# Kernel tuning notes

Measured on AMD Instinct MI355X. Metric: run time of the kernel, lower is better.

## Reference

```python
import jax, jax.numpy as jnp
import numpy as np
import math

B, N, M, Lx = 8, 32, 16, 32
D, TE_DIM, IN_DIM, TT = 64, 16, 17, 63   # hid_dim, te_dim, 1+te_dim, hid_dim-1
H, DH, NL = 4, 16, 2
TAU, DELTA = 60.0, 300.0                 # tau, 5 minutes in seconds
P = B * N * M


def _ln(x, g, b):
    mu = x.mean(-1, keepdims=True)
    v = ((x - mu) ** 2).mean(-1, keepdims=True)
    return (x - mu) / jnp.sqrt(v + 1e-5) * g + b


def _time_bias():
    idx = jnp.arange(M)
    dist = jnp.abs(idx[:, None] - idx[None, :]).astype(jnp.float32) * DELTA
    return jnp.log(jnp.exp(-dist / TAU) + 1e-12)


def _pos_enc():
    pos = jnp.arange(M, dtype=jnp.float32)[:, None]
    div = jnp.exp(jnp.arange(0, D, 2, dtype=jnp.float32) * (-math.log(10000.0) / D))
    pe = jnp.zeros((M, D))
    pe = pe.at[:, 0::2].set(jnp.sin(pos * div))
    pe = pe.at[:, 1::2].set(jnp.cos(pos * div))
    return pe


def _heads(t):   # (b, m, D) -> (b, H, m, DH)
    b, m, _ = t.shape
    return t.reshape(b, m, H, DH).transpose(0, 2, 1, 3)


def _merge(t):   # (b, H, m, DH) -> (b, m, D)
    b, _, m, _ = t.shape
    return t.transpose(0, 2, 1, 3).reshape(b, m, D)


def _patch_gattn(x, pm, qw, qb, kw, kb, vw, vb, ow, ob, tbias):
    q, k, v = _heads(x @ qw.T + qb), _heads(x @ kw.T + kb), _heads(x @ vw.T + vb)
    a = jnp.einsum('bhqd,bhkd->bhqk', q, k) / math.sqrt(DH) + tbias[None, None]
    a = jnp.where((pm == 0.0)[:, None, None, :], -1e9, a)
    out = _merge(jnp.einsum('bhqk,bhkd->bhqd', jax.nn.softmax(a, -1), v))
    return (out @ ow.T + ob) * pm[..., None]


def _mha(q_in, kv_in, in_w, in_b, ow, ob, kpm=None):
    wq, wk, wv = in_w[:D], in_w[D:2 * D], in_w[2 * D:]
    bq, bk, bv = in_b[:D], in_b[D:2 * D], in_b[2 * D:]
    q = _heads(q_in @ wq.T + bq)
    k = _heads(kv_in @ wk.T + bk)
    v = _heads(kv_in @ wv.T + bv)
    a = jnp.einsum('bhqd,bhkd->bhqk', q, k) / math.sqrt(DH)
    if kpm is not None:
        a = jnp.where(kpm[:, None, None, :], -1e9, a)
    out = _merge(jnp.einsum('bhqk,bhkd->bhqd', jax.nn.softmax(a, -1), v))
    return out @ ow.T + ob


def _forward(x, mask, ttcn_w1, ttcn_b1, ttcn_w2, ttcn_b2, ttcn_w3, ttcn_b3, t_bias,
             ga_qw, ga_qb, ga_kw, ga_kb, ga_vw, ga_vb, ga_ow, ga_ob,
             tf_in_w, tf_in_b, tf_out_w, tf_out_b, tf_ln1_g, tf_ln1_b, tf_ln2_g, tf_ln2_b,
             tf_fw1, tf_fb1, tf_fw2, tf_fb2,
             q_embed, cls_in_w, cls_in_b, cls_out_w, cls_out_b, logit_w, logit_b):
    m = mask.astype(x.dtype)                          # (P, Lx, 1)
    # --- TTCN: per-sample dynamic filter generation + masked seq-softmax agg ---
    h = jax.nn.relu(x @ ttcn_w1.T + ttcn_b1)
    h = jax.nn.relu(h @ ttcn_w2.T + ttcn_b2)
    filt = h @ ttcn_w3.T + ttcn_b3                    # (P, Lx, IN_DIM*TT)
    filt = filt * m + (1.0 - m) * (-1e8)
    fs = jax.nn.softmax(filt, axis=1).reshape(P, Lx, TT, IN_DIM)
    h_t = jax.nn.relu(jnp.einsum('pli,plti->pt', x, fs) + t_bias)   # (P, TT)
    mask_patch = (m.sum(axis=1) > 0).astype(x.dtype)  # (P, 1)
    xp = jnp.concatenate([h_t, mask_patch], -1).reshape(B, N, M, D)
    pm = mask_patch.reshape(B, N, M)
    tbias = _time_bias()
    pe = _pos_enc()
    xc = xp
    for l in range(NL):
        if l > 0:
            x_last = xc
        xb = xc.reshape(B * N, M, D)
        pmb = pm.reshape(B * N, M)
        xb = xb + _patch_gattn(xb, pmb, ga_qw[l], ga_qb[l], ga_kw[l], ga_kb[l],
                               ga_vw[l], ga_vb[l], ga_ow[l], ga_ob[l], tbias)
        xb = xb + pe[None]
        # post-norm TransformerEncoderLayer (tf_layer = 1, no attn mask, eval mode)
        attn = _mha(xb, xb, tf_in_w[l], tf_in_b[l], tf_out_w[l], tf_out_b[l])
        xb = _ln(xb + attn, tf_ln1_g[l], tf_ln1_b[l])
        ff = jax.nn.relu(xb @ tf_fw1[l].T + tf_fb1[l]) @ tf_fw2[l].T + tf_fb2[l]
        xb = _ln(xb + ff, tf_ln2_g[l], tf_ln2_b[l])
        xc = xb.reshape(B, N, M, D)
        if l > 0:
            xc = x_last + xc
    x_seq = xc.mean(axis=1)                            # (B, M, D)
    kpm = ~((pm > 0).any(axis=1))                      # (B, M), True = padded
    qs = jnp.broadcast_to(q_embed[None], (B, 5, D))
    z = _mha(qs, x_seq, cls_in_w, cls_in_b, cls_out_w, cls_out_b, kpm=kpm)
    return (z @ logit_w.T + logit_b)[..., 0]           # (B, 5)


def setup_inputs() -> dict:
    key = jax.random.key(0)
    ks = iter(jax.random.split(key, 64))
    def rn(shape, s=0.1):
        return jax.random.normal(next(ks), shape, jnp.float32) * s
    inp = {
        'x': jax.random.normal(next(ks), (P, Lx, IN_DIM), jnp.float32),
        'mask': jax.random.randint(next(ks), (P, Lx, 1), 0, 2, jnp.int32),
        'ttcn_w1': rn((TT, IN_DIM)), 'ttcn_b1': jnp.zeros((TT,)),
        'ttcn_w2': rn((TT, TT)), 'ttcn_b2': jnp.zeros((TT,)),
        'ttcn_w3': rn((IN_DIM * TT, TT)), 'ttcn_b3': jnp.zeros((IN_DIM * TT,)),
        't_bias': rn((1, TT)),
        'ga_qw': rn((NL, D, D)), 'ga_qb': jnp.zeros((NL, D)),
        'ga_kw': rn((NL, D, D)), 'ga_kb': jnp.zeros((NL, D)),
        'ga_vw': rn((NL, D, D)), 'ga_vb': jnp.zeros((NL, D)),
        'ga_ow': rn((NL, D, D)), 'ga_ob': jnp.zeros((NL, D)),
        'tf_in_w': rn((NL, 3 * D, D)), 'tf_in_b': jnp.zeros((NL, 3 * D)),
        'tf_out_w': rn((NL, D, D)), 'tf_out_b': jnp.zeros((NL, D)),
        'tf_ln1_g': jnp.ones((NL, D)), 'tf_ln1_b': jnp.zeros((NL, D)),
        'tf_ln2_g': jnp.ones((NL, D)), 'tf_ln2_b': jnp.zeros((NL, D)),
        'tf_fw1': rn((NL, 2048, D)), 'tf_fb1': jnp.zeros((NL, 2048)),
        'tf_fw2': rn((NL, D, 2048)), 'tf_fb2': jnp.zeros((NL, D)),
        'q_embed': rn((5, D), 1.0),
        'cls_in_w': rn((3 * D, D)), 'cls_in_b': jnp.zeros((3 * D,)),
        'cls_out_w': rn((D, D)), 'cls_out_b': jnp.zeros((D,)),
        'logit_w': rn((1, D)), 'logit_b': jnp.zeros((1,)),
    }
    return inp


def reference(x, mask, ttcn_w1, ttcn_b1, ttcn_w2, ttcn_b2, ttcn_w3, ttcn_b3, t_bias,
              ga_qw, ga_qb, ga_kw, ga_kb, ga_vw, ga_vb, ga_ow, ga_ob,
              tf_in_w, tf_in_b, tf_out_w, tf_out_b, tf_ln1_g, tf_ln1_b, tf_ln2_g, tf_ln2_b,
              tf_fw1, tf_fb1, tf_fw2, tf_fb2,
              q_embed, cls_in_w, cls_in_b, cls_out_w, cls_out_b, logit_w, logit_b):
    return _forward(x, mask, ttcn_w1, ttcn_b1, ttcn_w2, ttcn_b2, ttcn_w3, ttcn_b3, t_bias,
                    ga_qw, ga_qb, ga_kw, ga_kb, ga_vw, ga_vb, ga_ow, ga_ob,
                    tf_in_w, tf_in_b, tf_out_w, tf_out_b, tf_ln1_g, tf_ln1_b, tf_ln2_g, tf_ln2_b,
                    tf_fw1, tf_fb1, tf_fw2, tf_fb2,
                    q_embed, cls_in_w, cls_in_b, cls_out_w, cls_out_b, logit_w, logit_b)
```

## Files before the change

### kernel.cpp

```cpp
#include <hip/hip_runtime.h>
#include <hip/hip_bf16.h>
#include <math.h>

#define B_  8
#define N_  32
#define M_  16
#define LX  32
#define D_  64
#define IN_DIM_ 17
#define TT_ 63
#define H_  4
#define DH_ 16
#define P_TOT 4096
#define BN_ 256
#define FF_ 2048

#define FRAG_TOT 83200
#define OFF_INW  2048
#define OFF_OUTW 3584
#define OFF_FW1  4096
#define OFF_FW2  20480

typedef unsigned short ushort_t;
typedef __attribute__((ext_vector_type(8))) short short8;
typedef __attribute__((ext_vector_type(4))) float floatx4;

#define MFMA16(a,b,c) __builtin_amdgcn_mfma_f32_16x16x32_bf16((a),(b),(c),0,0,0)

__device__ __forceinline__ float fast_exp2(float x){
#if __has_builtin(__builtin_amdgcn_exp2f)
  return __builtin_amdgcn_exp2f(x);
#else
  return __expf(x * 0.6931471805599453f);
#endif
}
__device__ __forceinline__ float fast_rcp(float x){
#if __has_builtin(__builtin_amdgcn_rcpf)
  return __builtin_amdgcn_rcpf(x);
#else
  return 1.0f / x;
#endif
}

__device__ __forceinline__ ushort_t f2bf(float f){
  unsigned u = __float_as_uint(f);
  u += 0x7FFFu + ((u >> 16) & 1u);
  return (ushort_t)(u >> 16);
}
__device__ __forceinline__ float bf2f(ushort_t h){ return __uint_as_float(((unsigned)h) << 16); }

__device__ __forceinline__ uint4 pack8(const ushort_t* h){
  uint4 u;
  u.x = (unsigned)h[0] | ((unsigned)h[1] << 16);
  u.y = (unsigned)h[2] | ((unsigned)h[3] << 16);
  u.z = (unsigned)h[4] | ((unsigned)h[5] << 16);
  u.w = (unsigned)h[6] | ((unsigned)h[7] << 16);
  return u;
}

__device__ __forceinline__ void split8(const float* r, short8& hi, short8& lo){
  #pragma unroll
  for (int j = 0; j < 8; ++j){
    float v = r[j];
    ushort_t h = f2bf(v);
    ushort_t l2 = f2bf(v - bf2f(h));
    hi[j] = (short)h; lo[j] = (short)l2;
  }
}
__device__ __forceinline__ uint4 cvt8(const float* r){
  ushort_t hh[8];
  #pragma unroll
  for (int j = 0; j < 8; ++j) hh[j] = f2bf(r[j]);
  return pack8(hh);
}
__device__ __forceinline__ short8 cvt8s(const float* r){
  union { uint4 u4; short8 s8; } cv;
  cv.u4 = cvt8(r);
  return cv.s8;
}

__device__ __forceinline__ floatx4 mm3(short8 ah, short8 al, short8 bh, short8 bl, floatx4 c){
  c = MFMA16(ah, bh, c); c = MFMA16(ah, bl, c); c = MFMA16(al, bh, c); return c;
}

__device__ __forceinline__ float dot64(const float* __restrict__ a, const float* __restrict__ w){
  const float4* a4 = (const float4*)a;
  const float4* w4 = (const float4*)w;
  float acc = 0.f;
  #pragma unroll
  for (int k = 0; k < 16; ++k){ float4 x = a4[k], y = w4[k];
    acc += x.x*y.x + x.y*y.y + x.z*y.z + x.w*y.w; }
  return acc;
}
__device__ __forceinline__ float dot16(const float* __restrict__ a, const float* __restrict__ b){
  const float4* a4 = (const float4*)a; const float4* b4 = (const float4*)b;
  float acc = 0.f;
  #pragma unroll
  for (int k = 0; k < 4; ++k){ float4 x = a4[k], y = b4[k];
    acc += x.x*y.x + x.y*y.y + x.z*y.z + x.w*y.w; }
  return acc;
}

__device__ __forceinline__ void packA68(const float* buf, short8* fA, int tid){
  if (tid < 128){
    int ln = tid & 63, ks = tid >> 6;
    const float* r = buf + (ln & 15)*68 + ks*32 + ((ln >> 4) & 3)*8;
    short8 hi, lo; split8(r, hi, lo);
    fA[tid] = hi; fA[128 + tid] = lo;
  }
}

__global__ __launch_bounds__(256) void prep_kernel(
    const float* __restrict__ w1, const float* __restrict__ w2, const float* __restrict__ w3,
    const float* __restrict__ gqw, const float* __restrict__ gkw,
    const float* __restrict__ gvw, const float* __restrict__ gow,
    const float* __restrict__ inw, const float* __restrict__ outw,
    const float* __restrict__ fw1, const float* __restrict__ fw2,
    uint4* __restrict__ fr)
{
  int s = blockIdx.x*256 + threadIdx.x;
  if (s >= FRAG_TOT) return;
  const float* src; int Nr, Kr, KS, rel; int w3seg = 0, noLo = 0;
  if (s < 256)      { src = w1; Nr=63;  Kr=17; KS=1; rel = s; noLo = 1; }
  else if (s < 768) { src = w2; Nr=63;  Kr=63; KS=2; rel = s-256; noLo = 1; }
  else if (s < 9472){ src = w3; Nr=1071;Kr=63; KS=2; rel = s-768; w3seg = 1; noLo = 1; }
  else {
    int t = s - 9472, l = t / 36864, r2 = t - l*36864;
    if (r2 < 512)        { src = gqw + l*4096;   Nr=64;  Kr=64;   KS=2;  rel = r2; }
    else if (r2 < 1024)  { src = gkw + l*4096;   Nr=64;  Kr=64;   KS=2;  rel = r2-512; }
    else if (r2 < 1536)  { src = gvw + l*4096;   Nr=64;  Kr=64;   KS=2;  rel = r2-1024; }
    else if (r2 < 2048)  { src = gow + l*4096;   Nr=64;  Kr=64;   KS=2;  rel = r2-1536; }
    else if (r2 < 3584)  { src = inw + l*12288;  Nr=192; Kr=64;   KS=2;  rel = r2-2048; }
    else if (r2 < 4096)  { src = outw + l*4096;  Nr=64;  Kr=64;   KS=2;  rel = r2-3584; }
    else if (r2 < 20480) { src = fw1 + l*131072; Nr=2048;Kr=64;   KS=2;  rel = r2-4096; noLo = 1; }
    else                 { src = fw2 + l*131072; Nr=64;  Kr=2048; KS=64; rel = r2-20480; noLo = 1; }
  }
  int lane = rel & 63, tmp = rel >> 6;
  int ks = tmp % KS, nt = tmp / KS;
  int kb = ks*32 + ((lane >> 4) & 3)*8;
  int n, validn;
  if (w3seg){
    int i = nt >> 2, tq = nt & 3;
    int t = tq*16 + (lane & 15);
    n = t*17 + i;
    validn = (t < 63);
  } else {
    n = nt*16 + (lane & 15);
    validn = (n < Nr);
  }
  float v[8];
  #pragma unroll
  for (int j = 0; j < 8; ++j){
    v[j] = (validn && (kb + j) < Kr) ? src[n*Kr + kb + j] : 0.f;
    if (w3seg){
      if ((kb + j) == 63) v[j] = 1.0f;
      v[j] *= 1.4426950408889634f;
    }
  }
  ushort_t hh[8];
  #pragma unroll
  for (int j = 0; j < 8; ++j) hh[j] = f2bf(v[j]);
  fr[s] = pack8(hh);
  if (!noLo){
    ushort_t ll[8];
    #pragma unroll
    for (int j = 0; j < 8; ++j) ll[j] = f2bf(v[j] - bf2f(hh[j]));
    fr[FRAG_TOT + s] = pack8(ll);
  }
}

__global__ __launch_bounds__(256) void ttcn_kernel(
    const float* __restrict__ x, const int* __restrict__ mask,
    const float* __restrict__ b1, const float* __restrict__ b2,
    const float* __restrict__ tb,
    const short8* __restrict__ w1bhi,
    const short8* __restrict__ w2bhi,
    const short8* __restrict__ w3bhi,
    float* __restrict__ xp, float* __restrict__ pm)
{
  __shared__ __align__(16) char pool[16512];
  float*    xs    = (float*)(pool + 0);
  float*    xst   = (float*)(pool + 2560);
  int*      cmap  = (int*)  (pool + 5008);
  float*    xsumv = (float*)(pool + 5136);
  int*      Vp    = (int*)  (pool + 5204);
  short8*   xfhi  = (short8*)(pool + 5216);
  ushort_t* h1t   = (ushort_t*)(pool + 7264);
  ushort_t* h2t   = (ushort_t*)(pool + 11872);

  const int p = blockIdx.x, tid = threadIdx.x;
  const int lane = tid & 63, wvi = tid >> 6;
  const int nidx = lane & 15, quad = lane >> 4;

  for (int idx = tid; idx < LX*IN_DIM_; idx += 256){
    int l = (idx * 3856) >> 16;
    int i = idx - l*17;
    xs[l*20 + i] = x[p*(LX*IN_DIM_) + idx];
  }
  if (tid < 64){
    int mv = (tid < 32) ? mask[p*LX + tid] : 0;
    unsigned long long bal = __ballot(mv != 0);
    if (tid < 32) cmap[tid] = 0;
    int pos = __popcll(bal & ((1ull << tid) - 1ull));
    if (mv != 0) cmap[pos] = tid;
    if (tid == 0) *Vp = (int)__popcll(bal);
  }
  __syncthreads();
  const int V   = *Vp;
  const int two = (V > 16);

  if (tid < 128){
    int mt = tid >> 6;
    if (mt == 0 || two){
      int lc = cmap[mt*16 + nidx];
      float r[8];
      #pragma unroll
      for (int j = 0; j < 8; ++j){
        int k = quad*8 + j;
        r[j] = (k < IN_DIM_) ? xs[lc*20 + k] : 0.f;
      }
      ((uint4*)xfhi)[tid] = cvt8(r);
    }
  } else {
    if (tid < 128 + IN_DIM_){
      int i = tid - 128;
      float s = 0.f;
      #pragma unroll
      for (int l = 0; l < LX; ++l) s += xs[l*20 + i];
      xsumv[i] = s;
    }
    if (two){
      for (int idx = tid - 128; idx < 544; idx += 128){
        int i = idx >> 5, cl = idx & 31;
        xst[i*36 + cl] = xs[cmap[cl]*20 + i];
      }
    } else {
      for (int idx = tid - 128; idx < 272; idx += 128){
        int i = idx >> 4, cl = idx & 15;
        xst[i*36 + cl] = xs[cmap[cl]*20 + i];
      }
    }
  }
  __syncthreads();

  {
    short8 axh0 = xfhi[lane];
    short8 bh = w1bhi[wvi*64 + lane];
    floatx4 a0 = {0.f,0.f,0.f,0.f};
    a0 = MFMA16(axh0, bh, a0);
    int t = wvi*16 + nidx;
    float bb = (t < TT_) ? b1[t] : 0.f;
    if (two){
      short8 axh1 = xfhi[64 + lane];
      floatx4 a1 = {0.f,0.f,0.f,0.f};
      a1 = MFMA16(axh1, bh, a1);
      #pragma unroll
      for (int r = 0; r < 4; ++r)
        h1t[(16+quad*4+r)*72 + t] = f2bf(fmaxf(a1[r] + bb, 0.f));
    }
    #pragma unroll
    for (int r = 0; r < 4; ++r)
      h1t[(quad*4+r)*72 + t] = f2bf(fmaxf(a0[r] + bb, 0.f));
  }
  __syncthreads();

  {
    short8 bh0 = w2bhi[(wvi*2+0)*64 + lane];
    short8 bh1 = w2bhi[(wvi*2+1)*64 + lane];
    short8 a00 = *(const short8*)((const char*)h1t + (nidx*72 + quad*8)*2);
    short8 a01 = *(const short8*)((const char*)h1t + (nidx*72 + 32 + quad*8)*2);
    floatx4 a0 = {0.f,0.f,0.f,0.f};
    a0 = MFMA16(a00, bh0, a0); a0 = MFMA16(a01, bh1, a0);
    int t = wvi*16 + nidx;
    float bb = (t < TT_) ? b2[t] : 0.f;
    if (two){
      short8 a10 = *(const short8*)((const char*)h1t + ((16+nidx)*72 + quad*8)*2);
      short8 a11 = *(const short8*)((const char*)h1t + ((16+nidx)*72 + 32 + quad*8)*2);
      floatx4 a1 = {0.f,0.f,0.f,0.f};
      a1 = MFMA16(a10, bh0, a1); a1 = MFMA16(a11, bh1, a1);
      #pragma unroll
      for (int r = 0; r < 4; ++r)
        h2t[(16+quad*4+r)*72 + t] = f2bf(fmaxf(a1[r] + bb, 0.f));
    }
    #pragma unroll
    for (int r = 0; r < 4; ++r)
      h2t[(quad*4+r)*72 + t] = f2bf(fmaxf(a0[r] + bb, 0.f));
  }
  __syncthreads();

  {
    short8 ah0[2], ah1[2];
    #pragma unroll
    for (int ks = 0; ks < 2; ++ks)
      ah0[ks] = *(const short8*)((const char*)h2t + (nidx*72 + ks*32 + quad*8)*2);
    if (two){
      #pragma unroll
      for (int ks = 0; ks < 2; ++ks)
        ah1[ks] = *(const short8*)((const char*)h2t + ((16+nidx)*72 + ks*32 + quad*8)*2);
    }
    if (quad == 3){
      if (two) ah1[1][7] = (short)((16 + nidx >= V) ? f2bf(-1e8f) : (ushort_t)0);
      else     ah0[1][7] = (short)((nidx >= V)      ? f2bf(-1e8f) : (ushort_t)0);
    }
    const int t_out = wvi*16 + nidx;
    const int rA = quad*4;
    float acc_t = 0.f;
    short8 nbh0 = w3bhi[(wvi*2+0)*64 + lane];
    short8 nbh1 = w3bhi[(wvi*2+1)*64 + lane];
    if (two){
      for (int it = 0; it < 17; ++it){
        short8 bh0 = nbh0, bh1 = nbh1;
        if (it < 16){
          int nt = wvi + it*4 + 4;
          nbh0 = w3bhi[(nt*2+0)*64 + lane];
          nbh1 = w3bhi[(nt*2+1)*64 + lane];
        }
        floatx4 a0 = {0.f,0.f,0.f,0.f}, a1 = {0.f,0.f,0.f,0.f};
        a0 = MFMA16(ah0[0], bh0, a0); a0 = MFMA16(ah0[1], bh1, a0);
        a1 = MFMA16(ah1[0], bh0, a1); a1 = MFMA16(ah1[1], bh1, a1);

        const float4 xA = *(const float4*)(xst + it*36 + rA);
        const float4 xB = *(const float4*)(xst + it*36 + rA + 16);
        float den0 = 0.f, den1 = 0.f, num0 = 0.f, num1 = 0.f;
        float e;
        e = fast_exp2(a0[0]); den0 += e; num0 = fmaf(e, xA.x, num0);
        e = fast_exp2(a0[1]); den0 += e; num0 = fmaf(e, xA.y, num0);
        e = fast_exp2(a0[2]); den0 += e; num0 = fmaf(e, xA.z, num0);
        e = fast_exp2(a0[3]); den0 += e; num0 = fmaf(e, xA.w, num0);
        e = fast_exp2(a1[0]); den1 += e; num1 = fmaf(e, xB.x, num1);
        e = fast_exp2(a1[1]); den1 += e; num1 = fmaf(e, xB.y, num1);
        e = fast_exp2(a1[2]); den1 += e; num1 = fmaf(e, xB.z, num1);
        e = fast_exp2(a1[3]); den1 += e; num1 = fmaf(e, xB.w, num1);
        float den = den0 + den1, num = num0 + num1;
        den += __shfl_xor(den, 16, 64); den += __shfl_xor(den, 32, 64);
        num += __shfl_xor(num, 16, 64); num += __shfl_xor(num, 32, 64);
        float res = (den > 0.f) ? num * fast_rcp(den) : xsumv[it] * (1.f/32.f);
        acc_t += res;
      }
    } else {
      for (int it = 0; it < 17; ++it){
        short8 bh0 = nbh0, bh1 = nbh1;
        if (it < 16){
          int nt = wvi + it*4 + 4;
          nbh0 = w3bhi[(nt*2+0)*64 + lane];
          nbh1 = w3bhi[(nt*2+1)*64 + lane];
        }
        floatx4 a0 = {0.f,0.f,0.f,0.f};
        a0 = MFMA16(ah0[0], bh0, a0); a0 = MFMA16(ah0[1], bh1, a0);

        const float4 xA = *(const float4*)(xst + it*36 + rA);
        float den = 0.f, num = 0.f, e;
        e = fast_exp2(a0[0]); den += e; num = fmaf(e, xA.x, num);
        e = fast_exp2(a0[1]); den += e; num = fmaf(e, xA.y, num);
        e = fast_exp2(a0[2]); den += e; num = fmaf(e, xA.z, num);
        e = fast_exp2(a0[3]); den += e; num = fmaf(e, xA.w, num);
        den += __shfl_xor(den, 16, 64); den += __shfl_xor(den, 32, 64);
        num += __shfl_xor(num, 16, 64); num += __shfl_xor(num, 32, 64);
        float res = (den > 0.f) ? num * fast_rcp(den) : xsumv[it] * (1.f/32.f);
        acc_t += res;
      }
    }
    if (quad == 0 && t_out < TT_)
      xp[p*D_ + t_out] = fmaxf(acc_t + tb[t_out], 0.f);
  }
  if (tid == 0){
    float mp = (V > 0) ? 1.f : 0.f;
    xp[p*D_ + TT_] = mp;
    pm[p] = mp;
  }
}

__global__ __launch_bounds__(512) void layer12_kernel(
    const float* __restrict__ xin, const float* __restrict__ pm,
    const short8* __restrict__ frS,
    const float* __restrict__ gqb, const float* __restrict__ gkb,
    const float* __restrict__ gvb, const float* __restrict__ gob,
    const float* __restrict__ inb, const float* __restrict__ outb,
    const float* __restrict__ ln1g, const float* __restrict__ ln1b,
    const float* __restrict__ fb1, const float* __restrict__ fb2,
    const float* __restrict__ ln2g, const float* __restrict__ ln2b,
    float* __restrict__ xout)
{
  __shared__ __align__(16) float xb[16*68];
  __shared__ __align__(16) float xb2[16*68];
  __shared__ __align__(16) float q_[16*68];
  __shared__ __align__(16) float k_[16*68];
  __shared__ __align__(16) float v_[16*68];
  __shared__ __align__(16) float ao[16*68];
  __shared__ __align__(16) float ss[1024];
  __shared__ __align__(16) short8 fragA[256];
  __shared__ __align__(16) float hbuf[8*16*36];
  __shared__ __align__(16) float part[8*16*68];
  __shared__ __align__(16) float pe_t[1024];
  __shared__ float tbt[16];
  __shared__ float pmv[16], mur[16], rvr[16];

  const int bn = blockIdx.x, tid = threadIdx.x;
  const int lane = tid & 63, wvi = tid >> 6;
  const int nidx = lane & 15, quad = lane >> 4;
  const float* xin_p = xin + bn*1024;

  for (int o = tid; o < 1024; o += 512) xb[(o>>6)*68 + (o&63)] = xin_p[o];
  if (tid < 16) pmv[tid] = pm[bn*16 + tid];
  for (int o = tid; o < 1024; o += 512){
    int tok = o >> 6, d = o & 63;
    float div = __expf((float)(d & ~1) * (-0.14391156831212793f));
    float arg = (float)tok * div;
    pe_t[o] = (d & 1) ? cosf(arg) : sinf(arg);
  }
  if (tid >= 32 && tid < 48) tbt[tid-32] = logf(expf(-5.0f*(float)(tid-32)) + 1e-12f);
  __syncthreads();

  for (int l = 0; l < 2; ++l){
    const int lbase = 9472 + l*36864;
    const float* gqbL = gqb + l*64;  const float* gkbL = gkb + l*64;
    const float* gvbL = gvb + l*64;  const float* gobL = gob + l*64;
    const float* inbL = inb + l*192; const float* outbL = outb + l*64;
    const float* ln1gL = ln1g + l*64; const float* ln1bL = ln1b + l*64;
    const float* fb1L = fb1 + l*2048; const float* fb2L = fb2 + l*64;
    const float* ln2gL = ln2g + l*64; const float* ln2bL = ln2b + l*64;

    float xres[2];
    #pragma unroll
    for (int kk2 = 0; kk2 < 2; ++kk2){
      int o = tid + kk2*512;
      xres[kk2] = xb[(o>>6)*68 + (o&63)];
    }

    short8 gU0[4], gU1[4], mU0[4], mU1[4], ob4[4];
    {
      int b0 = lbase + wvi*128;
      gU0[0] = frS[b0 + lane];       gU0[1] = frS[FRAG_TOT + b0 + lane];
      gU0[2] = frS[b0 + 64 + lane];  gU0[3] = frS[FRAG_TOT + b0 + 64 + lane];
      int m0 = lbase + OFF_INW + wvi*128;
      mU0[0] = frS[m0 + lane];       mU0[1] = frS[FRAG_TOT + m0 + lane];
      mU0[2] = frS[m0 + 64 + lane];  mU0[3] = frS[FRAG_TOT + m0 + 64 + lane];
      if (wvi < 4){
        int b1 = lbase + (wvi+8)*128;
        gU1[0] = frS[b1 + lane];       gU1[1] = frS[FRAG_TOT + b1 + lane];
        gU1[2] = frS[b1 + 64 + lane];  gU1[3] = frS[FRAG_TOT + b1 + 64 + lane];
        int m1 = lbase + OFF_INW + (wvi+8)*128;
        mU1[0] = frS[m1 + lane];       mU1[1] = frS[FRAG_TOT + m1 + lane];
        mU1[2] = frS[m1 + 64 + lane];  mU1[3] = frS[FRAG_TOT + m1 + 64 + lane];
        int bo = lbase + 1536 + wvi*128;
        ob4[0] = frS[bo + lane];       ob4[1] = frS[FRAG_TOT + bo + lane];
        ob4[2] = frS[bo + 64 + lane];  ob4[3] = frS[FRAG_TOT + bo + 64 + lane];
      }
    }

    packA68(xb, fragA, tid);
    __syncthreads();
    {
      short8 axh0 = fragA[lane], axh1 = fragA[64+lane];
      short8 axl0 = fragA[128+lane], axl1 = fragA[192+lane];
      {
        int u = wvi;
        floatx4 c = {0.f,0.f,0.f,0.f};
        c = mm3(axh0, axl0, gU0[0], gU0[1], c);
        c = mm3(axh1, axl1, gU0[2], gU0[3], c);
        int sel = u >> 2, d = (u & 3)*16 + nidx;
        float bb = (sel == 0 ? gqbL : gkbL)[d];
        float* dst = (sel == 0 ? q_ : k_);
        #pragma unroll
        for (int r = 0; r < 4; ++r) dst[(quad*4+r)*68 + d] = c[r] + bb;
      }
      if (wvi < 4){
        int u = wvi + 8;
        floatx4 c = {0.f,0.f,0.f,0.f};
        c = mm3(axh0, axl0, gU1[0], gU1[1], c);
        c = mm3(axh1, axl1, gU1[2], gU1[3], c);
        int d = (u & 3)*16 + nidx;
        float bb = gvbL[d];
        #pragma unroll
        for (int r = 0; r < 4; ++r) v_[(quad*4+r)*68 + d] = c[r] + bb;
      }
    }
    __syncthreads();
    {
      int row = tid >> 3;
      int h = row >> 4, qm = row & 15;
      int km0 = (tid & 7) * 2;
      float s2[2];
      #pragma unroll
      for (int j = 0; j < 2; ++j){
        int km = km0 + j;
        float acc = dot16(q_ + qm*68 + h*16, k_ + km*68 + h*16);
        int dd = qm - km; if (dd < 0) dd = -dd;
        acc = acc * 0.25f + tbt[dd];
        if (pmv[km] == 0.f) acc = -1e9f;
        s2[j] = acc;
      }
      float mx = fmaxf(s2[0], s2[1]);
      mx = fmaxf(mx, __shfl_xor(mx, 1, 64));
      mx = fmaxf(mx, __shfl_xor(mx, 2, 64));
      mx = fmaxf(mx, __shfl_xor(mx, 4, 64));
      float e2[2], se = 0.f;
      #pragma unroll
      for (int j = 0; j < 2; ++j){ e2[j] = __expf(s2[j]-mx); se += e2[j]; }
      se += __shfl_xor(se, 1, 64);
      se += __shfl_xor(se, 2, 64);
      se += __shfl_xor(se, 4, 64);
      float inv = fast_rcp(se);
      #pragma unroll
      for (int j = 0; j < 2; ++j) ss[row*16 + km0 + j] = e2[j]*inv;
    }
    __syncthreads();
    for (int o = tid; o < 1024; o += 512){
      int m = o >> 6, d = o & 63, h = d >> 4;
      float acc = 0.f;
      #pragma unroll
      for (int km = 0; km < 16; ++km) acc += ss[h*256 + m*16 + km] * v_[km*68 + d];
      ao[m*68 + d] = acc;
    }
    __syncthreads();
    packA68(ao, fragA, tid);
    __syncthreads();
    if (wvi < 4){
      short8 axh0 = fragA[lane], axh1 = fragA[64+lane];
      short8 axl0 = fragA[128+lane], axl1 = fragA[192+lane];
      floatx4 c = {0.f,0.f,0.f,0.f};
      c = mm3(axh0, axl0, ob4[0], ob4[1], c);
      c = mm3(axh1, axl1, ob4[2], ob4[3], c);
      int d = wvi*16 + nidx;
      float bb = gobL[d];
      #pragma unroll
      for (int r = 0; r < 4; ++r){
        int tok = quad*4 + r;
        xb[tok*68 + d] += (c[r] + bb) * pmv[tok] + pe_t[tok*64 + d];
      }
    }
    __syncthreads();

    short8 mob[4], f1c[4], f2c[4];
    if (wvi < 4){
      int base = lbase + OFF_OUTW + wvi*128;
      mob[0] = frS[base + lane];       mob[1] = frS[FRAG_TOT + base + lane];
      mob[2] = frS[base + 64 + lane];  mob[3] = frS[FRAG_TOT + base + 64 + lane];
    }
    {
      int f1base = lbase + OFF_FW1, f2base = lbase + OFF_FW2;
      #pragma unroll
      for (int t2 = 0; t2 < 2; ++t2){
        int sb = f1base + ((wvi*16+t2)*2)*64 + lane;
        f1c[t2*2+0] = frS[sb];
        f1c[t2*2+1] = frS[sb + 64];
      }
      #pragma unroll
      for (int ntd = 0; ntd < 4; ++ntd)
        f2c[ntd] = frS[f2base + (ntd*64 + wvi*8)*64 + lane];
    }

    packA68(xb, fragA, tid);
    __syncthreads();
    {
      short8 axh0 = fragA[lane], axh1 = fragA[64+lane];
      short8 axl0 = fragA[128+lane], axl1 = fragA[192+lane];
      {
        int u = wvi;
        floatx4 c = {0.f,0.f,0.f,0.f};
        c = mm3(axh0, axl0, mU0[0], mU0[1], c);
        c = mm3(axh1, axl1, mU0[2], mU0[3], c);
        int sel = u >> 2, d = (u & 3)*16 + nidx;
        float bb = inbL[u*16 + nidx];
        float* dst = (sel == 0 ? q_ : k_);
        #pragma unroll
        for (int r = 0; r < 4; ++r) dst[(quad*4+r)*68 + d] = c[r] + bb;
      }
      if (wvi < 4){
        int u = wvi + 8;
        floatx4 c = {0.f,0.f,0.f,0.f};
        c = mm3(axh0, axl0, mU1[0], mU1[1], c);
        c = mm3(axh1, axl1, mU1[2], mU1[3], c);
        int d = (u & 3)*16 + nidx;
        float bb = inbL[u*16 + nidx];
        #pragma unroll
        for (int r = 0; r < 4; ++r) v_[(quad*4+r)*68 + d] = c[r] + bb;
      }
    }
    __syncthreads();
    {
      int row = tid >> 3;
      int h = row >> 4, qm = row & 15;
      int km0 = (tid & 7) * 2;
      float s2[2];
      #pragma unroll
      for (int j = 0; j < 2; ++j)
        s2[j] = 0.25f * dot16(q_ + qm*68 + h*16, k_ + (km0+j)*68 + h*16);
      float mx = fmaxf(s2[0], s2[1]);
      mx = fmaxf(mx, __shfl_xor(mx, 1, 64));
      mx = fmaxf(mx, __shfl_xor(mx, 2, 64));
      mx = fmaxf(mx, __shfl_xor(mx, 4, 64));
      float e2[2], se = 0.f;
      #pragma unroll
      for (int j = 0; j < 2; ++j){ e2[j] = __expf(s2[j]-mx); se += e2[j]; }
      se += __shfl_xor(se, 1, 64);
      se += __shfl_xor(se, 2, 64);
      se += __shfl_xor(se, 4, 64);
      float inv = fast_rcp(se);
      #pragma unroll
      for (int j = 0; j < 2; ++j) ss[row*16 + km0 + j] = e2[j]*inv;
    }
    __syncthreads();
    for (int o = tid; o < 1024; o += 512){
      int m = o >> 6, d = o & 63, h = d >> 4;
      float acc = 0.f;
      #pragma unroll
      for (int km = 0; km < 16; ++km) acc += ss[h*256 + m*16 + km] * v_[km*68 + d];
      ao[m*68 + d] = acc;
    }
    __syncthreads();
    packA68(ao, fragA, tid);
    __syncthreads();
    if (wvi < 4){
      short8 axh0 = fragA[lane], axh1 = fragA[64+lane];
      short8 axl0 = fragA[128+lane], axl1 = fragA[192+lane];
      floatx4 c = {0.f,0.f,0.f,0.f};
      c = mm3(axh0, axl0, mob[0], mob[1], c);
      c = mm3(axh1, axl1, mob[2], mob[3], c);
      int d = wvi*16 + nidx;
      float bb = outbL[d];
      #pragma unroll
      for (int r = 0; r < 4; ++r) xb[(quad*4+r)*68 + d] += c[r] + bb;
    }
    __syncthreads();

    if (tid < 64){
      int row = tid >> 2, seg = tid & 3;
      const float* rp = xb + row*68 + seg*16;
      float s = 0.f;
      #pragma unroll
      for (int j = 0; j < 16; ++j) s += rp[j];
      s += __shfl_xor(s, 1, 64); s += __shfl_xor(s, 2, 64);
      float mu = s * (1.f/64.f);
      float v = 0.f;
      #pragma unroll
      for (int j = 0; j < 16; ++j){ float t = rp[j]-mu; v += t*t; }
      v += __shfl_xor(v, 1, 64); v += __shfl_xor(v, 2, 64);
      if (seg == 0){ mur[row] = mu; rvr[row] = rsqrtf(v*(1.f/64.f) + 1e-5f); }
    }
    __syncthreads();
    for (int o = tid; o < 1024; o += 512){
      int m = o >> 6, d = o & 63;
      xb2[m*68 + d] = (xb[m*68 + d] - mur[m]) * rvr[m] * ln1gL[d] + ln1bL[d];
    }
    __syncthreads();
    packA68(xb2, fragA, tid);
    __syncthreads();

    {
      const int w = wvi;
      const int f1base = lbase + OFF_FW1, f2base = lbase + OFF_FW2;
      short8 axh0 = fragA[lane], axh1 = fragA[64 + lane];
      floatx4 y0 = {0.f,0.f,0.f,0.f}, y1 = y0, y2 = y0, y3 = y0;
      float* hw = hbuf + w*576;

      short8 f1n[4], f2n[4];
      for (int it = 0; it < 8; ++it){
        int ntA = w*16 + it*2;
        floatx4 hA = {0.f,0.f,0.f,0.f}, hB = hA;
        hA = MFMA16(axh0, f1c[0], hA); hA = MFMA16(axh1, f1c[1], hA);
        hB = MFMA16(axh0, f1c[2], hB); hB = MFMA16(axh1, f1c[3], hB);
        float bbA = fb1L[ntA*16 + nidx], bbB = fb1L[ntA*16 + 16 + nidx];
        #pragma unroll
        for (int r = 0; r < 4; ++r){
          hw[(quad*4+r)*36 + nidx]      = fmaxf(hA[r] + bbA, 0.f);
          hw[(quad*4+r)*36 + 16 + nidx] = fmaxf(hB[r] + bbB, 0.f);
        }
        if (it < 7){
          int ntN = ntA + 2, kstN = w*8 + it + 1;
          #pragma unroll
          for (int t2 = 0; t2 < 2; ++t2){
            int sb = f1base + ((ntN+t2)*2)*64 + lane;
            f1n[t2*2+0] = frS[sb];
            f1n[t2*2+1] = frS[sb + 64];
          }
          #pragma unroll
          for (int ntd = 0; ntd < 4; ++ntd)
            f2n[ntd] = frS[f2base + (ntd*64 + kstN)*64 + lane];
        }
        short8 ah = cvt8s(hw + (lane & 15)*36 + quad*8);
        y0 = MFMA16(ah, f2c[0], y0);
        y1 = MFMA16(ah, f2c[1], y1);
        y2 = MFMA16(ah, f2c[2], y2);
        y3 = MFMA16(ah, f2c[3], y3);
        #pragma unroll
        for (int j = 0; j < 4; ++j){ f1c[j] = f1n[j]; f2c[j] = f2n[j]; }
      }
      #pragma unroll
      for (int r = 0; r < 4; ++r){
        int row = (quad*4 + r)*68;
        part[w*1088 + row + nidx]      = y0[r];
        part[w*1088 + row + 16 + nidx] = y1[r];
        part[w*1088 + row + 32 + nidx] = y2[r];
        part[w*1088 + row + 48 + nidx] = y3[r];
      }
    }
    __syncthreads();
    for (int o = tid; o < 1024; o += 512){
      int tok = o >> 6, d = o & 63;
      float s = xb2[tok*68 + d] + fb2L[d];
      #pragma unroll
      for (int ww = 0; ww < 8; ++ww) s += part[ww*1088 + tok*68 + d];
      xb[tok*68 + d] = s;
    }
    __syncthreads();
    if (tid < 64){
      int row = tid >> 2, seg = tid & 3;
      const float* rp = xb + row*68 + seg*16;
      float s = 0.f;
      #pragma unroll
      for (int j = 0; j < 16; ++j) s += rp[j];
      s += __shfl_xor(s, 1, 64); s += __shfl_xor(s, 2, 64);
      float mu = s * (1.f/64.f);
      float v = 0.f;
      #pragma unroll
      for (int j = 0; j < 16; ++j){ float t = rp[j]-mu; v += t*t; }
      v += __shfl_xor(v, 1, 64); v += __shfl_xor(v, 2, 64);
      if (seg == 0){ mur[row] = mu; rvr[row] = rsqrtf(v*(1.f/64.f) + 1e-5f); }
    }
    __syncthreads();
    #pragma unroll
    for (int kk2 = 0; kk2 < 2; ++kk2){
      int o = tid + kk2*512;
      int tok = o >> 6, d = o & 63;
      float vv = (xb[tok*68 + d] - mur[tok]) * rvr[tok] * ln2gL[d] + ln2bL[d];
      if (l == 0) xb[tok*68 + d] = vv;
      else        xout[bn*1024 + o] = vv + xres[kk2];
    }
    __syncthreads();
  }
}

__global__ __launch_bounds__(256) void final_kernel(
    const float* __restrict__ xc, const float* __restrict__ pm,
    const float* __restrict__ q_embed,
    const float* __restrict__ cin_w, const float* __restrict__ cin_b,
    const float* __restrict__ cout_w, const float* __restrict__ cout_b,
    const float* __restrict__ logit_w, const float* __restrict__ logit_b,
    float* __restrict__ out)
{
  const int b = blockIdx.x;
  const int tid = threadIdx.x;
  __shared__ __align__(16) float xs[M_ * D_];
  __shared__ float kpmv[M_];
  __shared__ __align__(16) float qv[5 * D_], kv[M_ * D_], vv[M_ * D_];
  __shared__ float sv[H_ * 5 * M_];
  __shared__ __align__(16) float ao[5 * D_], zv[5 * D_];

  for (int o = tid; o < M_ * D_; o += 256) {
    int m = o >> 6, d = o & 63;
    float acc = 0.f;
    #pragma unroll
    for (int n = 0; n < N_; ++n) acc += xc[(((b * N_ + n) * M_ + m) * D_) + d];
    xs[o] = acc * (1.f / 32.f);
  }
  if (tid < M_) {
    float any = 0.f;
    #pragma unroll
    for (int n = 0; n < N_; ++n) any += (pm[(b * N_ + n) * M_ + tid] > 0.f) ? 1.f : 0.f;
    kpmv[tid] = (any > 0.f) ? 0.f : 1.f;
  }
  __syncthreads();

  for (int o = tid; o < 5 * D_; o += 256) {
    int qi = o >> 6, d = o & 63;
    qv[o] = cin_b[d] + dot64(q_embed + qi * D_, cin_w + d * D_);
  }
  for (int o = tid; o < 2 * M_ * D_; o += 256) {
    int sel = o >> 10, r = o & 1023, m = r >> 6, d = r & 63;
    float acc = cin_b[D_ + sel * D_ + d] + dot64(xs + m * D_, cin_w + (D_ + sel * D_ + d) * D_);
    ((sel == 0) ? kv : vv)[r] = acc;
  }
  __syncthreads();

  for (int o = tid; o < H_ * 5 * M_; o += 256) {
    int h = o / 80, r = o % 80, qi = r >> 4, km = r & 15;
    float acc = 0.25f * dot16(qv + qi * D_ + h * DH_, kv + km * D_ + h * DH_);
    if (kpmv[km] != 0.f) acc = -1e9f;
    sv[o] = acc;
  }
  __syncthreads();
  if (tid < H_ * 5) {
    int h = tid / 5, qi = tid % 5;
    float* row = sv + h * 80 + qi * M_;
    float mx = -1e30f;
    #pragma unroll
    for (int km = 0; km < M_; ++km) mx = fmaxf(mx, row[km]);
    float se = 0.f;
    #pragma unroll
    for (int km = 0; km < M_; ++km) { float e = __expf(row[km] - mx); row[km] = e; se += e; }
    float inv = 1.f / se;
    #pragma unroll
    for (int km = 0; km < M_; ++km) row[km] *= inv;
  }
  __syncthreads();
  for (int o = tid; o < 5 * D_; o += 256) {
    int qi = o >> 6, d = o & 63, h = d >> 4;
    float acc = 0.f;
    #pragma unroll
    for (int km = 0; km < M_; ++km) acc += sv[h * 80 + qi * M_ + km] * vv[km * D_ + d];
    ao[o] = acc;
  }
  __syncthreads();
  for (int o = tid; o < 5 * D_; o += 256) {
    int qi = o >> 6, d = o & 63;
    zv[o] = cout_b[d] + dot64(ao + qi * D_, cout_w + d * D_);
  }
  __syncthreads();
  if (tid < 5) {
    float acc = logit_b[0] + dot64(zv + tid * D_, logit_w);
    out[b * 5 + tid] = acc;
  }
}

extern "C" void kernel_launch(void* const* d_in, const int* in_sizes, int n_in,
                              void* d_out, int out_size, void* d_ws, size_t ws_size,
                              hipStream_t stream) {
  const float* x       = (const float*)d_in[0];
  const int*   mask    = (const int*)  d_in[1];
  const float* ttcn_w1 = (const float*)d_in[2];
  const float* ttcn_b1 = (const float*)d_in[3];
  const float* ttcn_w2 = (const float*)d_in[4];
  const float* ttcn_b2 = (const float*)d_in[5];
  const float* ttcn_w3 = (const float*)d_in[6];
  const float* ttcn_b3 = (const float*)d_in[7];
  const float* t_bias  = (const float*)d_in[8];
  const float* ga_qw   = (const float*)d_in[9];
  const float* ga_qb   = (const float*)d_in[10];
  const float* ga_kw   = (const float*)d_in[11];
  const float* ga_kb   = (const float*)d_in[12];
  const float* ga_vw   = (const float*)d_in[13];
  const float* ga_vb   = (const float*)d_in[14];
  const float* ga_ow   = (const float*)d_in[15];
  const float* ga_ob   = (const float*)d_in[16];
  const float* tf_in_w = (const float*)d_in[17];
  const float* tf_in_b = (const float*)d_in[18];
  const float* tf_out_w= (const float*)d_in[19];
  const float* tf_out_b= (const float*)d_in[20];
  const float* tf_ln1g = (const float*)d_in[21];
  const float* tf_ln1b = (const float*)d_in[22];
  const float* tf_ln2g = (const float*)d_in[23];
  const float* tf_ln2b = (const float*)d_in[24];
  const float* tf_fw1  = (const float*)d_in[25];
  const float* tf_fb1  = (const float*)d_in[26];
  const float* tf_fw2  = (const float*)d_in[27];
  const float* tf_fb2  = (const float*)d_in[28];
  const float* q_embed = (const float*)d_in[29];
  const float* cls_in_w  = (const float*)d_in[30];
  const float* cls_in_b  = (const float*)d_in[31];
  const float* cls_out_w = (const float*)d_in[32];
  const float* cls_out_b = (const float*)d_in[33];
  const float* logit_w = (const float*)d_in[34];
  const float* logit_b = (const float*)d_in[35];
  (void)ttcn_b3;

  float* wsf  = (float*)d_ws;
  float* xp   = wsf;
  float* pmb  = wsf + P_TOT * D_;
  float* xbuf = pmb + P_TOT;
  uint4* fr   = (uint4*)(xbuf + P_TOT * D_);
  const short8* frS = (const short8*)fr;

  prep_kernel<<<325, 256, 0, stream>>>(ttcn_w1, ttcn_w2, ttcn_w3,
      ga_qw, ga_kw, ga_vw, ga_ow, tf_in_w, tf_out_w, tf_fw1, tf_fw2, fr);

  ttcn_kernel<<<P_TOT, 256, 0, stream>>>(x, mask, ttcn_b1, ttcn_b2, t_bias,
      frS + 0, frS + 256, frS + 768,
      xp, pmb);

  layer12_kernel<<<BN_, 512, 0, stream>>>(xp, pmb, frS,
      ga_qb, ga_kb, ga_vb, ga_ob, tf_in_b, tf_out_b, tf_ln1g, tf_ln1b,
      tf_fb1, tf_fb2, tf_ln2g, tf_ln2b, xbuf);

  final_kernel<<<B_, 256, 0, stream>>>(xbuf, pmb, q_embed,
                                       cls_in_w, cls_in_b, cls_out_w, cls_out_b,
                                       logit_w, logit_b, (float*)d_out);
}
```

Baseline: 229.2 us.

## Double ttcn block width to split work across wave groups; wave-level LayerNorm

The ttcn kernel now runs 512 threads per patch. Two groups of four waves split the work: in the first two layers each group handles one 16-row tile, and in the third-layer loop each group handles about half the iterations. The partial sums are combined through shared memory after an extra barrier. In layer12, both LayerNorms become per-wave 64-lane shuffle reductions over whole rows, which drops the separate mean/rstd shared-memory pass and two barriers. This adds parallelism and cuts synchronization, at the cost of idle waves when only one row tile is valid and possibly lower occupancy.

```diff
diff --git a/kernel.cpp b/kernel.cpp
--- a/kernel.cpp
+++ b/kernel.cpp
@@ -108,6 +108,13 @@
     short8 hi, lo; split8(r, hi, lo);
     fA[tid] = hi; fA[128 + tid] = lo;
   }
+}
+
+__device__ __forceinline__ float wsum64(float v){
+  v += __shfl_xor(v, 1, 64);  v += __shfl_xor(v, 2, 64);
+  v += __shfl_xor(v, 4, 64);  v += __shfl_xor(v, 8, 64);
+  v += __shfl_xor(v, 16, 64); v += __shfl_xor(v, 32, 64);
+  return v;
 }
 
 __global__ __launch_bounds__(256) void prep_kernel(
@@ -169,7 +176,7 @@
   }
 }
 
-__global__ __launch_bounds__(256) void ttcn_kernel(
+__global__ __launch_bounds__(512) void ttcn_kernel(
     const float* __restrict__ x, const int* __restrict__ mask,
     const float* __restrict__ b1, const float* __restrict__ b2,
     const float* __restrict__ tb,
@@ -187,12 +194,14 @@
   short8*   xfhi  = (short8*)(pool + 5216);
   ushort_t* h1t   = (ushort_t*)(pool + 7264);
   ushort_t* h2t   = (ushort_t*)(pool + 11872);
+  __shared__ float accp[64];
 
   const int p = blockIdx.x, tid = threadIdx.x;
   const int lane = tid & 63, wvi = tid >> 6;
+  const int w4 = wvi & 3, grp = wvi >> 2;
   const int nidx = lane & 15, quad = lane >> 4;
 
-  for (int idx = tid; idx < LX*IN_DIM_; idx += 256){
+  for (int idx = tid; idx < LX*IN_DIM_; idx += 512){
     int l = (idx * 3856) >> 16;
     int i = idx - l*17;
     xs[l*20 + i] = x[p*(LX*IN_DIM_) + idx];
@@ -230,12 +239,12 @@
       xsumv[i] = s;
     }
     if (two){
-      for (int idx = tid - 128; idx < 544; idx += 128){
+      for (int idx = tid - 128; idx < 544; idx += 384){
         int i = idx >> 5, cl = idx & 31;
         xst[i*36 + cl] = xs[cmap[cl]*20 + i];
       }
     } else {
-      for (int idx = tid - 128; idx < 272; idx += 128){
+      for (int idx = tid - 128; idx < 272; idx += 384){
         int i = idx >> 4, cl = idx & 15;
         xst[i*36 + cl] = xs[cmap[cl]*20 + i];
       }
@@ -244,13 +253,17 @@
   __syncthreads();
 
   {
-    short8 axh0 = xfhi[lane];
-    short8 bh = w1bhi[wvi*64 + lane];
-    floatx4 a0 = {0.f,0.f,0.f,0.f};
-    a0 = MFMA16(axh0, bh, a0);
-    int t = wvi*16 + nidx;
+    int t = w4*16 + nidx;
     float bb = (t < TT_) ? b1[t] : 0.f;
-    if (two){
+    short8 bh = w1bhi[w4*64 + lane];
+    if (grp == 0){
+      short8 axh0 = xfhi[lane];
+      floatx4 a0 = {0.f,0.f,0.f,0.f};
+      a0 = MFMA16(axh0, bh, a0);
+      #pragma unroll
+      for (int r = 0; r < 4; ++r)
+        h1t[(quad*4+r)*72 + t] = f2bf(fmaxf(a0[r] + bb, 0.f));
+    } else if (two){
       short8 axh1 = xfhi[64 + lane];
       floatx4 a1 = {0.f,0.f,0.f,0.f};
       a1 = MFMA16(axh1, bh, a1);
@@ -258,22 +271,23 @@
       for (int r = 0; r < 4; ++r)
         h1t[(16+quad*4+r)*72 + t] = f2bf(fmaxf(a1[r] + bb, 0.f));
     }
-    #pragma unroll
-    for (int r = 0; r < 4; ++r)
-      h1t[(quad*4+r)*72 + t] = f2bf(fmaxf(a0[r] + bb, 0.f));
   }
   __syncthreads();
 
   {
-    short8 bh0 = w2bhi[(wvi*2+0)*64 + lane];
-    short8 bh1 = w2bhi[(wvi*2+1)*64 + lane];
-    short8 a00 = *(const short8*)((const char*)h1t + (nidx*72 + quad*8)*2);
-    short8 a01 = *(const short8*)((const char*)h1t + (nidx*72 + 32 + quad*8)*2);
-    floatx4 a0 = {0.f,0.f,0.f,0.f};
-    a0 = MFMA16(a00, bh0, a0); a0 = MFMA16(a01, bh1, a0);
-    int t = wvi*16 + nidx;
+    int t = w4*16 + nidx;
     float bb = (t < TT_) ? b2[t] : 0.f;
-    if (two){
+    short8 bh0 = w2bhi[(w4*2+0)*64 + lane];
+    short8 bh1 = w2bhi[(w4*2+1)*64 + lane];
+    if (grp == 0){
+      short8 a00 = *(const short8*)((const char*)h1t + (nidx*72 + quad*8)*2);
+      short8 a01 = *(const short8*)((const char*)h1t + (nidx*72 + 32 + quad*8)*2);
+      floatx4 a0 = {0.f,0.f,0.f,0.f};
+      a0 = MFMA16(a00, bh0, a0); a0 = MFMA16(a01, bh1, a0);
+      #pragma unroll
+      for (int r = 0; r < 4; ++r)
+        h2t[(quad*4+r)*72 + t] = f2bf(fmaxf(a0[r] + bb, 0.f));
+    } else if (two){
       short8 a10 = *(const short8*)((const char*)h1t + ((16+nidx)*72 + quad*8)*2);
       short8 a11 = *(const short8*)((const char*)h1t + ((16+nidx)*72 + 32 + quad*8)*2);
       floatx4 a1 = {0.f,0.f,0.f,0.f};
@@ -282,9 +296,6 @@
       for (int r = 0; r < 4; ++r)
         h2t[(16+quad*4+r)*72 + t] = f2bf(fmaxf(a1[r] + bb, 0.f));
     }
-    #pragma unroll
-    for (int r = 0; r < 4; ++r)
-      h2t[(quad*4+r)*72 + t] = f2bf(fmaxf(a0[r] + bb, 0.f));
   }
   __syncthreads();
 
@@ -302,16 +313,16 @@
       if (two) ah1[1][7] = (short)((16 + nidx >= V) ? f2bf(-1e8f) : (ushort_t)0);
       else     ah0[1][7] = (short)((nidx >= V)      ? f2bf(-1e8f) : (ushort_t)0);
     }
-    const int t_out = wvi*16 + nidx;
+    const int it0 = grp ? 9 : 0, it1 = grp ? 17 : 9;
     const int rA = quad*4;
     float acc_t = 0.f;
-    short8 nbh0 = w3bhi[(wvi*2+0)*64 + lane];
-    short8 nbh1 = w3bhi[(wvi*2+1)*64 + lane];
+    short8 nbh0 = w3bhi[((w4 + it0*4)*2+0)*64 + lane];
+    short8 nbh1 = w3bhi[((w4 + it0*4)*2+1)*64 + lane];
     if (two){
-      for (int it = 0; it < 17; ++it){
+      for (int it = it0; it < it1; ++it){
         short8 bh0 = nbh0, bh1 = nbh1;
-        if (it < 16){
-          int nt = wvi + it*4 + 4;
+        if (it + 1 < 17){
+          int nt = w4 + it*4 + 4;
           nbh0 = w3bhi[(nt*2+0)*64 + lane];
           nbh1 = w3bhi[(nt*2+1)*64 + lane];
         }
@@ -338,10 +349,10 @@
         acc_t += res;
       }
     } else {
-      for (int it = 0; it < 17; ++it){
+      for (int it = it0; it < it1; ++it){
         short8 bh0 = nbh0, bh1 = nbh1;
-        if (it < 16){
-          int nt = wvi + it*4 + 4;
+        if (it + 1 < 17){
+          int nt = w4 + it*4 + 4;
           nbh0 = w3bhi[(nt*2+0)*64 + lane];
           nbh1 = w3bhi[(nt*2+1)*64 + lane];
         }
@@ -360,8 +371,13 @@
         acc_t += res;
       }
     }
-    if (quad == 0 && t_out < TT_)
-      xp[p*D_ + t_out] = fmaxf(acc_t + tb[t_out], 0.f);
+    if (grp == 1 && quad == 0) accp[w4*16 + nidx] = acc_t;
+    __syncthreads();
+    if (grp == 0 && quad == 0){
+      int t_out = w4*16 + nidx;
+      if (t_out < TT_)
+        xp[p*D_ + t_out] = fmaxf(acc_t + accp[t_out] + tb[t_out], 0.f);
+    }
   }
   if (tid == 0){
     float mp = (V > 0) ? 1.f : 0.f;
@@ -393,7 +409,7 @@
   __shared__ __align__(16) float part[8*16*68];
   __shared__ __align__(16) float pe_t[1024];
   __shared__ float tbt[16];
-  __shared__ float pmv[16], mur[16], rvr[16];
+  __shared__ float pmv[16];
 
   const int bn = blockIdx.x, tid = threadIdx.x;
   const int lane = tid & 63, wvi = tid >> 6;
@@ -421,11 +437,8 @@
     const float* ln2gL = ln2g + l*64; const float* ln2bL = ln2b + l*64;
 
     float xres[2];
-    #pragma unroll
-    for (int kk2 = 0; kk2 < 2; ++kk2){
-      int o = tid + kk2*512;
-      xres[kk2] = xb[(o>>6)*68 + (o&63)];
-    }
+    xres[0] = xb[wvi*68 + lane];
+    xres[1] = xb[(wvi+8)*68 + lane];
 
     short8 gU0[4], gU1[4], mU0[4], mU1[4], ob4[4];
     {
@@ -624,24 +637,17 @@
     }
     __syncthreads();
 
-    if (tid < 64){
-      int row = tid >> 2, seg = tid & 3;
-      const float* rp = xb + row*68 + seg*16;
-      float s = 0.f;
-      #pragma unroll
-      for (int j = 0; j < 16; ++j) s += rp[j];
-      s += __shfl_xor(s, 1, 64); s += __shfl_xor(s, 2, 64);
-      float mu = s * (1.f/64.f);
-      float v = 0.f;
-      #pragma unroll
-      for (int j = 0; j < 16; ++j){ float t = rp[j]-mu; v += t*t; }
-      v += __shfl_xor(v, 1, 64); v += __shfl_xor(v, 2, 64);
-      if (seg == 0){ mur[row] = mu; rvr[row] = rsqrtf(v*(1.f/64.f) + 1e-5f); }
-    }
-    __syncthreads();
-    for (int o = tid; o < 1024; o += 512){
-      int m = o >> 6, d = o & 63;
-      xb2[m*68 + d] = (xb[m*68 + d] - mur[m]) * rvr[m] * ln1gL[d] + ln1bL[d];
+    {
+      float a = xb[wvi*68 + lane], b = xb[(wvi+8)*68 + lane];
+      float mua = wsum64(a) * (1.f/64.f);
+      float mub = wsum64(b) * (1.f/64.f);
+      float da = a - mua, db = b - mub;
+      float va = wsum64(da*da) * (1.f/64.f);
+      float vb = wsum64(db*db) * (1.f/64.f);
+      float rva = rsqrtf(va + 1e-5f), rvb = rsqrtf(vb + 1e-5f);
+      float g = ln1gL[lane], bia = ln1bL[lane];
+      xb2[wvi*68 + lane]     = da*rva*g + bia;
+      xb2[(wvi+8)*68 + lane] = db*rvb*g + bia;
     }
     __syncthreads();
     packA68(xb2, fragA, tid);
@@ -696,36 +702,30 @@
       }
     }
     __syncthreads();
-    for (int o = tid; o < 1024; o += 512){
-      int tok = o >> 6, d = o & 63;
-      float s = xb2[tok*68 + d] + fb2L[d];
-      #pragma unroll
-      for (int ww = 0; ww < 8; ++ww) s += part[ww*1088 + tok*68 + d];
-      xb[tok*68 + d] = s;
-    }
-    __syncthreads();
-    if (tid < 64){
-      int row = tid >> 2, seg = tid & 3;
-      const float* rp = xb + row*68 + seg*16;
-      float s = 0.f;
-      #pragma unroll
-      for (int j = 0; j < 16; ++j) s += rp[j];
-      s += __shfl_xor(s, 1, 64); s += __shfl_xor(s, 2, 64);
-      float mu = s * (1.f/64.f);
-      float v = 0.f;
-      #pragma unroll
-      for (int j = 0; j < 16; ++j){ float t = rp[j]-mu; v += t*t; }
-      v += __shfl_xor(v, 1, 64); v += __shfl_xor(v, 2, 64);
-      if (seg == 0){ mur[row] = mu; rvr[row] = rsqrtf(v*(1.f/64.f) + 1e-5f); }
-    }
-    __syncthreads();
-    #pragma unroll
-    for (int kk2 = 0; kk2 < 2; ++kk2){
-      int o = tid + kk2*512;
-      int tok = o >> 6, d = o & 63;
-      float vv = (xb[tok*68 + d] - mur[tok]) * rvr[tok] * ln2gL[d] + ln2bL[d];
-      if (l == 0) xb[tok*68 + d] = vv;
-      else        xout[bn*1024 + o] = vv + xres[kk2];
+    {
+      float ra = xb2[wvi*68 + lane] + fb2L[lane];
+      float rb = xb2[(wvi+8)*68 + lane] + fb2L[lane];
+      #pragma unroll
+      for (int ww = 0; ww < 8; ++ww){
+        ra += part[ww*1088 + wvi*68 + lane];
+        rb += part[ww*1088 + (wvi+8)*68 + lane];
+      }
+      float mua = wsum64(ra) * (1.f/64.f);
+      float mub = wsum64(rb) * (1.f/64.f);
+      float da = ra - mua, db = rb - mub;
+      float va = wsum64(da*da) * (1.f/64.f);
+      float vb = wsum64(db*db) * (1.f/64.f);
+      float rva = rsqrtf(va + 1e-5f), rvb = rsqrtf(vb + 1e-5f);
+      float g = ln2gL[lane], bia = ln2bL[lane];
+      float vva = da*rva*g + bia;
+      float vvb = db*rvb*g + bia;
+      if (l == 0){
+        xb[wvi*68 + lane]     = vva;
+        xb[(wvi+8)*68 + lane] = vvb;
+      } else {
+        xout[bn*1024 + wvi*64 + lane]     = vva + xres[0];
+        xout[bn*1024 + (wvi+8)*64 + lane] = vvb + xres[1];
+      }
     }
     __syncthreads();
   }
@@ -864,7 +864,7 @@
   prep_kernel<<<325, 256, 0, stream>>>(ttcn_w1, ttcn_w2, ttcn_w3,
       ga_qw, ga_kw, ga_vw, ga_ow, tf_in_w, tf_out_w, tf_fw1, tf_fw2, fr);
 
-  ttcn_kernel<<<P_TOT, 256, 0, stream>>>(x, mask, ttcn_b1, ttcn_b2, t_bias,
+  ttcn_kernel<<<P_TOT, 512, 0, stream>>>(x, mask, ttcn_b1, ttcn_b2, t_bias,
       frS + 0, frS + 256, frS + 768,
       xp, pmb);
 
```

New measurement: 232.8 us. Within noise of the previous version (+1.6%).
